# Optimization experiments

Measured on AMD Instinct MI355X. Metric: run time of the kernel, lower is better.

Reference implementation:

```python
import jax, jax.numpy as jnp
import numpy as np

B, S, D = 4, 2048, 768
H = 12
HD = D // H  # 64


def setup_inputs() -> dict:
    key = jax.random.key(0)
    k1, k2, k3 = jax.random.split(key, 3)
    return {
        "hidden_states": jax.random.normal(k1, (B, S, D), dtype=jnp.float32),
        "W_attn": jax.random.normal(k2, (D, 3 * D), dtype=jnp.float32) * 0.02,
        "b_attn": jnp.zeros((3 * D,), dtype=jnp.float32),
        "W_proj": jax.random.normal(k3, (D, D), dtype=jnp.float32) * 0.02,
        "b_proj": jnp.zeros((D,), dtype=jnp.float32),
    }


def reference(hidden_states, W_attn, b_attn, W_proj, b_proj):
    # Conv1D c_attn: x @ W + b -> [B, S, 3D]
    qkv = hidden_states @ W_attn + b_attn
    q, k, v = jnp.split(qkv, 3, axis=-1)

    def split_heads(t):
        # [B, S, D] -> [B, H, S, HD]
        return t.reshape(B, S, H, HD).transpose(0, 2, 1, 3)

    q, k, v = split_heads(q), split_heads(k), split_heads(v)

    # attn_weights = q @ k^T / sqrt(head_dim); NOTE: this module variant applies
    # no causal mask when attention_mask is None (faithful to source _attn).
    scale = jnp.asarray(HD, dtype=q.dtype) ** 0.5
    scores = jnp.einsum("bhqd,bhkd->bhqk", q, k) / scale
    weights = jax.nn.softmax(scores, axis=-1)

    attn = jnp.einsum("bhqk,bhkd->bhqd", weights, v)
    # merge heads -> [B, S, D]
    attn = attn.transpose(0, 2, 1, 3).reshape(B, S, D)
    # Conv1D c_proj
    out = attn @ W_proj + b_proj
    return out
```

## Files before the change

### kernel.cpp

```cpp
#include <hip/hip_runtime.h>

typedef short short8 __attribute__((ext_vector_type(8)));
typedef float f32x2 __attribute__((ext_vector_type(2)));
typedef float f32x4 __attribute__((ext_vector_type(4)));
typedef float f32x16 __attribute__((ext_vector_type(16)));

__device__ __forceinline__ unsigned short f2bf(float f){
  union { float f; unsigned int u; } x; x.f = f;
  unsigned int r = x.u + 0x7fffu + ((x.u >> 16) & 1u);
  return (unsigned short)(r >> 16);
}

__device__ __forceinline__ void gload_lds16(const void* g, void* l){
  __builtin_amdgcn_global_load_lds(
      (const __attribute__((address_space(1))) void*)g,
      (__attribute__((address_space(3))) void*)l, 16, 0, 0);
}

__device__ __forceinline__ unsigned int cvtpk_bf16(float lo, float hi){
  unsigned int r;
  asm("v_cvt_pk_bf16_f32 %0, %1, %2" : "=v"(r) : "v"(lo), "v"(hi));
  return r;
}

__device__ __forceinline__ f32x2 pk_add(f32x2 a, f32x2 b){
  f32x2 d;
  asm("v_pk_add_f32 %0, %1, %2" : "=v"(d) : "v"(a), "v"(b));
  return d;
}

__global__ __launch_bounds__(256) void prep_fused(const float* __restrict__ hs,
                                                  unsigned short* __restrict__ hbf,
                                                  const float* __restrict__ Wa,
                                                  unsigned short* __restrict__ WaT,
                                                  const float* __restrict__ Wp,
                                                  unsigned short* __restrict__ WpT){
  __shared__ float tile[64][68];
  const int b = blockIdx.x;
  const int t = threadIdx.x;
  if (b < 2048){
    const int n4 = 8192 * 768 / 4;
    int i = b * 256 + t;
    for (; i < n4; i += 2048 * 256){
      float4 v = ((const float4*)hs)[i];
      ushort4 o;
      o.x = f2bf(v.x); o.y = f2bf(v.y); o.z = f2bf(v.z); o.w = f2bf(v.w);
      ((ushort4*)hbf)[i] = o;
    }
    return;
  }
  const float* W; unsigned short* WT; int K, N, n0, k0;
  if (b < 2480){
    const int idx = b - 2048;
    W = Wa; WT = WaT; K = 768; N = 2304;
    n0 = (idx % 36) * 64; k0 = (idx / 36) * 64;
  } else {
    const int idx = b - 2480;
    W = Wp; WT = WpT; K = 768; N = 768;
    n0 = (idx % 12) * 64; k0 = (idx / 12) * 64;
  }
  const int qn = (t & 15) * 4;
  #pragma unroll
  for (int i = 0; i < 4; ++i){
    const int kk = (t >> 4) + i * 16;
    float4 v = *(const float4*)&W[(size_t)(k0 + kk) * N + n0 + qn];
    tile[kk][qn + 0] = v.x; tile[kk][qn + 1] = v.y;
    tile[kk][qn + 2] = v.z; tile[kk][qn + 3] = v.w;
  }
  __syncthreads();
  const int qk = (t & 15) * 4;
  #pragma unroll
  for (int i = 0; i < 4; ++i){
    const int nn = (t >> 4) + i * 16;
    ushort4 o;
    o.x = f2bf(tile[qk + 0][nn]); o.y = f2bf(tile[qk + 1][nn]);
    o.z = f2bf(tile[qk + 2][nn]); o.w = f2bf(tile[qk + 3][nn]);
    *(ushort4*)&WT[(size_t)(n0 + nn) * K + k0 + qk] = o;
  }
}

__global__ __launch_bounds__(256) void gemm_qkv(const unsigned short* __restrict__ A,
                                                const unsigned short* __restrict__ Bt,
                                                const float* __restrict__ bias,
                                                unsigned short* __restrict__ qkv){
  __shared__ unsigned short As[2][128 * 32];
  __shared__ unsigned short Bs[2][128 * 32];
  const int tid = threadIdx.x;
  const int wave = tid >> 6, lane = tid & 63;
  const int g = lane >> 4, l15 = lane & 15;
  const int wr = wave >> 1, wc = wave & 1;
  const int d = blockIdx.x;
  const int w = (d & 7) * 144 + (d >> 3);
  const int m0 = (w / 18) * 128, n0 = (w % 18) * 128;

  f32x4 acc[4][4] = {};

  auto stage = [&](int bi, int kt){
    const int k0 = kt * 32;
    #pragma unroll
    for (int c = 0; c < 2; ++c){
      const int z = c * 4096 + tid * 16;
      const int r = z >> 6;
      const int ys = (z & 63) ^ ((r & 3) << 4);
      gload_lds16((const char*)A + ((size_t)(m0 + r) * 768 + k0) * 2 + ys,
                  (char*)&As[bi][0] + c * 4096 + wave * 1024);
      gload_lds16((const char*)Bt + ((size_t)(n0 + r) * 768 + k0) * 2 + ys,
                  (char*)&Bs[bi][0] + c * 4096 + wave * 1024);
    }
  };

  stage(0, 0);
  for (int kt = 0; kt < 24; ++kt){
    __syncthreads();
    if (kt + 1 < 24) stage((kt + 1) & 1, kt + 1);
    const char* Ab = (const char*)&As[kt & 1][0];
    const char* Bb = (const char*)&Bs[kt & 1][0];
    short8 a[4], b[4];
    #pragma unroll
    for (int mt = 0; mt < 4; ++mt){
      const int row = wr * 64 + mt * 16 + l15;
      a[mt] = *(const short8*)(Ab + row * 64 + ((g * 16) ^ ((row & 3) << 4)));
    }
    #pragma unroll
    for (int nt = 0; nt < 4; ++nt){
      const int row = wc * 64 + nt * 16 + l15;
      b[nt] = *(const short8*)(Bb + row * 64 + ((g * 16) ^ ((row & 3) << 4)));
    }
    #pragma unroll
    for (int mt = 0; mt < 4; ++mt)
      #pragma unroll
      for (int nt = 0; nt < 4; ++nt)
        acc[mt][nt] = __builtin_amdgcn_mfma_f32_16x16x32_bf16(a[mt], b[nt], acc[mt][nt], 0, 0, 0);
  }

  #pragma unroll
  for (int nt = 0; nt < 4; ++nt){
    const int n = n0 + wc * 64 + nt * 16 + l15;
    const int which = n / 768;
    const float bs = bias[n];
    if (which == 2){
      const int hd = n & 63;
      const int head = (n - 1536) >> 6;
      #pragma unroll
      for (int mt = 0; mt < 4; ++mt){
        const int m = m0 + wr * 64 + mt * 16 + 4 * g;
        const int bb = m >> 11, sidx = m & 2047;
        unsigned short* dst = qkv + (size_t)2 * 6291456 +
                              ((size_t)(bb * 12 + head) * 64 + hd) * 2048 + sidx;
        #pragma unroll
        for (int rp = 0; rp < 2; ++rp){
          const unsigned int lo = f2bf(acc[mt][nt][2 * rp] + bs);
          const unsigned int hi = f2bf(acc[mt][nt][2 * rp + 1] + bs);
          *(unsigned int*)(dst + 2 * rp) = lo | (hi << 16);
        }
      }
    } else {
      const int h2 = (n - which * 768) >> 6;
      const int hd = n & 63;
      const float sc = (which == 0) ? 0.18033688f : 1.0f;
      #pragma unroll
      for (int mt = 0; mt < 4; ++mt)
        #pragma unroll
        for (int r = 0; r < 4; ++r){
          const int m = m0 + wr * 64 + mt * 16 + 4 * g + r;
          const int bb = m >> 11, sidx = m & 2047;
          qkv[(size_t)which * 6291456u +
              ((((size_t)bb * 12 + h2) * 2048 + sidx) * 64 + hd)] = f2bf((acc[mt][nt][r] + bs) * sc);
        }
    }
  }
}

__global__ __launch_bounds__(256) void gemm_proj(const unsigned short* __restrict__ A,
                                                 const unsigned short* __restrict__ Bt,
                                                 const float* __restrict__ bias,
                                                 float* __restrict__ out){
  __shared__ unsigned short As[2][128 * 32];
  __shared__ unsigned short Bs[2][64 * 32];
  const int tid = threadIdx.x;
  const int wave = tid >> 6, lane = tid & 63;
  const int g = lane >> 4, l15 = lane & 15;
  const int d = blockIdx.x;
  const int w = (d & 7) * 96 + (d >> 3);
  const int m0 = (w / 12) * 128, n0 = (w % 12) * 64;

  f32x4 acc[2][4] = {};

  auto stage = [&](int bi, int kt){
    const int k0 = kt * 32;
    #pragma unroll
    for (int c = 0; c < 2; ++c){
      const int z = c * 4096 + tid * 16;
      const int r = z >> 6;
      const int ys = (z & 63) ^ ((r & 3) << 4);
      gload_lds16((const char*)A + ((size_t)(m0 + r) * 768 + k0) * 2 + ys,
                  (char*)&As[bi][0] + c * 4096 + wave * 1024);
    }
    const int z = tid * 16;
    const int r = z >> 6;
    const int ys = (z & 63) ^ ((r & 3) << 4);
    gload_lds16((const char*)Bt + ((size_t)(n0 + r) * 768 + k0) * 2 + ys,
                (char*)&Bs[bi][0] + wave * 1024);
  };

  stage(0, 0);
  for (int kt = 0; kt < 24; ++kt){
    __syncthreads();
    if (kt + 1 < 24) stage((kt + 1) & 1, kt + 1);
    const char* Ab = (const char*)&As[kt & 1][0];
    const char* Bb = (const char*)&Bs[kt & 1][0];
    short8 a[2], b[4];
    #pragma unroll
    for (int mt = 0; mt < 2; ++mt){
      const int row = wave * 32 + mt * 16 + l15;
      a[mt] = *(const short8*)(Ab + row * 64 + ((g * 16) ^ ((row & 3) << 4)));
    }
    #pragma unroll
    for (int nt = 0; nt < 4; ++nt){
      const int row = nt * 16 + l15;
      b[nt] = *(const short8*)(Bb + row * 64 + ((g * 16) ^ ((row & 3) << 4)));
    }
    #pragma unroll
    for (int mt = 0; mt < 2; ++mt)
      #pragma unroll
      for (int nt = 0; nt < 4; ++nt)
        acc[mt][nt] = __builtin_amdgcn_mfma_f32_16x16x32_bf16(a[mt], b[nt], acc[mt][nt], 0, 0, 0);
  }

  #pragma unroll
  for (int mt = 0; mt < 2; ++mt)
    #pragma unroll
    for (int nt = 0; nt < 4; ++nt){
      const int n = n0 + nt * 16 + l15;
      const float bs = bias[n];
      #pragma unroll
      for (int r = 0; r < 4; ++r){
        const int m = m0 + wave * 32 + mt * 16 + 4 * g + r;
        out[(size_t)m * 768 + n] = acc[mt][nt][r] + bs;
      }
    }
}

__global__ __launch_bounds__(256) void attn_fwd7(const unsigned short* __restrict__ qw,
                                                 const unsigned short* __restrict__ kw,
                                                 const unsigned short* __restrict__ vtw,
                                                 unsigned short* __restrict__ aout){
  __shared__ unsigned short Ks[2][64 * 64];
  __shared__ unsigned short Vs[2][64 * 64];
  const int tid = threadIdx.x;
  const int wave = tid >> 6, lane = tid & 63;
  const int h = lane >> 5, ql = lane & 31;
  const int dd = blockIdx.x;
  const int wk = (dd & 7) * 96 + (dd >> 3);
  const int bh = wk >> 4;
  const int q0 = (wk & 15) * 128 + wave * 32;
  const size_t base = (size_t)bh * 2048 * 64;

  short8 qf[4];
  #pragma unroll
  for (int c = 0; c < 4; ++c)
    qf[c] = *(const short8*)(qw + base + (size_t)(q0 + ql) * 64 + c * 16 + h * 8);

  f32x16 acc[2] = {};
  float lsum = 0.f;

  auto stageKV = [&](int bi, int t){
    #pragma unroll
    for (int c = 0; c < 2; ++c){
      const int z = c * 4096 + tid * 16;
      const int r = z >> 7, y = z & 127;
      const int ys = y ^ ((r & 7) << 4);
      gload_lds16((const char*)kw + (base + (size_t)(t * 64 + r) * 64) * 2 + ys,
                  (char*)&Ks[bi][0] + z);
      gload_lds16((const char*)vtw + (base + (size_t)r * 2048 + t * 64) * 2 + ys,
                  (char*)&Vs[bi][0] + z);
    }
  };

  stageKV(0, 0);
  __syncthreads();

  for (int t = 0; t < 32; ++t){
    const int buf = t & 1;
    if (t + 1 < 32) stageKV(buf ^ 1, t + 1);

    f32x16 s[2] = {};
    #pragma unroll
    for (int kt = 0; kt < 2; ++kt)
      #pragma unroll
      for (int c = 0; c < 4; ++c){
        const int row = kt * 32 + ql;
        short8 af = *(const short8*)((const char*)&Ks[buf][0] + row * 128 +
                                     ((c * 32 + h * 16) ^ ((row & 7) << 4)));
        s[kt] = __builtin_amdgcn_mfma_f32_32x32x16_bf16(af, qf[c], s[kt], 0, 0, 0);
      }

    #pragma unroll
    for (int kt = 0; kt < 2; ++kt)
      #pragma unroll
      for (int r = 0; r < 16; ++r)
        s[kt][r] = __builtin_amdgcn_exp2f(s[kt][r]);

    {
      f32x2 a0 = pk_add(__builtin_shufflevector(s[0], s[0], 0, 1),  __builtin_shufflevector(s[0], s[0], 2, 3));
      f32x2 a1 = pk_add(__builtin_shufflevector(s[0], s[0], 4, 5),  __builtin_shufflevector(s[0], s[0], 6, 7));
      f32x2 a2 = pk_add(__builtin_shufflevector(s[0], s[0], 8, 9),  __builtin_shufflevector(s[0], s[0], 10, 11));
      f32x2 a3 = pk_add(__builtin_shufflevector(s[0], s[0], 12, 13), __builtin_shufflevector(s[0], s[0], 14, 15));
      f32x2 b0 = pk_add(__builtin_shufflevector(s[1], s[1], 0, 1),  __builtin_shufflevector(s[1], s[1], 2, 3));
      f32x2 b1 = pk_add(__builtin_shufflevector(s[1], s[1], 4, 5),  __builtin_shufflevector(s[1], s[1], 6, 7));
      f32x2 b2 = pk_add(__builtin_shufflevector(s[1], s[1], 8, 9),  __builtin_shufflevector(s[1], s[1], 10, 11));
      f32x2 b3 = pk_add(__builtin_shufflevector(s[1], s[1], 12, 13), __builtin_shufflevector(s[1], s[1], 14, 15));
      a0 = pk_add(a0, a1); a2 = pk_add(a2, a3);
      b0 = pk_add(b0, b1); b2 = pk_add(b2, b3);
      a0 = pk_add(a0, a2); b0 = pk_add(b0, b2);
      a0 = pk_add(a0, b0);
      lsum += a0[0] + a0[1];
    }

    #pragma unroll
    for (int kt = 0; kt < 2; ++kt){
      unsigned int w0 = cvtpk_bf16(s[kt][0],  s[kt][1]),  x0 = cvtpk_bf16(s[kt][4],  s[kt][5]);
      asm("v_permlane32_swap_b32 %0, %1" : "+v"(w0), "+v"(x0));
      unsigned int w1 = cvtpk_bf16(s[kt][2],  s[kt][3]),  x1 = cvtpk_bf16(s[kt][6],  s[kt][7]);
      asm("v_permlane32_swap_b32 %0, %1" : "+v"(w1), "+v"(x1));
      unsigned int w2 = cvtpk_bf16(s[kt][8],  s[kt][9]),  x2 = cvtpk_bf16(s[kt][12], s[kt][13]);
      asm("v_permlane32_swap_b32 %0, %1" : "+v"(w2), "+v"(x2));
      unsigned int w3 = cvtpk_bf16(s[kt][10], s[kt][11]), x3 = cvtpk_bf16(s[kt][14], s[kt][15]);
      asm("v_permlane32_swap_b32 %0, %1" : "+v"(w3), "+v"(x3));
      union { unsigned int u[4]; short8 v; } pa2[2];
      pa2[0].u[0] = w0; pa2[0].u[1] = w1; pa2[0].u[2] = x0; pa2[0].u[3] = x1;
      pa2[1].u[0] = w2; pa2[1].u[1] = w3; pa2[1].u[2] = x2; pa2[1].u[3] = x3;
      #pragma unroll
      for (int c2 = 0; c2 < 2; ++c2){
        const int kc = kt * 2 + c2;
        #pragma unroll
        for (int ht = 0; ht < 2; ++ht){
          const int row = ht * 32 + ql;
          short8 vb = *(const short8*)((const char*)&Vs[buf][0] + row * 128 +
                                       ((kc * 32 + h * 16) ^ ((row & 7) << 4)));
          acc[ht] = __builtin_amdgcn_mfma_f32_32x32x16_bf16(pa2[c2].v, vb, acc[ht], 0, 0, 0);
        }
      }
    }

    __syncthreads();
  }

  lsum += __shfl_xor(lsum, 32);
  const float inv = 1.0f / lsum;
  const int bb = bh / 12, hh = bh % 12;
  #pragma unroll
  for (int g4 = 0; g4 < 4; ++g4)
    #pragma unroll
    for (int j = 0; j < 4; ++j){
      const int row = 8 * g4 + 4 * h + j;
      const float li = __shfl(inv, row);
      #pragma unroll
      for (int ht = 0; ht < 2; ++ht)
        aout[(size_t)(bb * 2048 + q0 + row) * 768 + hh * 64 + ht * 32 + ql] =
            f2bf(acc[ht][4 * g4 + j] * li);
    }
}

extern "C" void kernel_launch(void* const* d_in, const int* in_sizes, int n_in,
                              void* d_out, int out_size, void* d_ws, size_t ws_size,
                              hipStream_t stream){
  const float* hs = (const float*)d_in[0];
  const float* Wa = (const float*)d_in[1];
  const float* ba = (const float*)d_in[2];
  const float* Wp = (const float*)d_in[3];
  const float* bp = (const float*)d_in[4];

  char* ws = (char*)d_ws;
  unsigned short* hbf = (unsigned short*)ws;
  unsigned short* WaT = (unsigned short*)(ws + 12582912);
  unsigned short* WpT = (unsigned short*)(ws + 12582912 + 3538944);
  unsigned short* qkv = (unsigned short*)(ws + 12582912 + 3538944 + 1179648);
  unsigned short* abf = qkv + (size_t)3 * 6291456;

  prep_fused<<<dim3(2624), dim3(256), 0, stream>>>(hs, hbf, Wa, WaT, Wp, WpT);
  gemm_qkv<<<dim3(1152), dim3(256), 0, stream>>>(hbf, WaT, ba, qkv);
  attn_fwd7<<<dim3(768), dim3(256), 0, stream>>>(qkv, qkv + 6291456, qkv + (size_t)2 * 6291456, abf);
  gemm_proj<<<dim3(768), dim3(256), 0, stream>>>(abf, WpT, bp, (float*)d_out);
}
```

Measured before the change: 151.6 us.

## Split QKV GEMM into QK and transposed-output V kernels, change LDS swizzle

The fused QKV projection is split into a Q/K GEMM and a separate V GEMM. The V GEMM swaps operand roles so the accumulator comes out transposed, which lets the transposed V layout be written along the sequence dimension with contiguous lanes. The attention kernel's K/V LDS swizzle now XORs in higher row bits to reduce bank conflicts. The cost is an extra kernel launch, and the V path now does scalar 2-byte stores instead of packed 4-byte stores.

```diff
diff --git a/kernel.cpp b/kernel.cpp
--- a/kernel.cpp
+++ b/kernel.cpp
@@ -27,6 +27,10 @@
   f32x2 d;
   asm("v_pk_add_f32 %0, %1, %2" : "=v"(d) : "v"(a), "v"(b));
   return d;
+}
+
+__device__ __forceinline__ int kvswz(int r){
+  return (((r & 7) ^ ((r >> 3) & 7)) << 4);
 }
 
 __global__ __launch_bounds__(256) void prep_fused(const float* __restrict__ hs,
@@ -79,10 +83,10 @@
   }
 }
 
-__global__ __launch_bounds__(256) void gemm_qkv(const unsigned short* __restrict__ A,
-                                                const unsigned short* __restrict__ Bt,
-                                                const float* __restrict__ bias,
-                                                unsigned short* __restrict__ qkv){
+__global__ __launch_bounds__(256) void gemm_qk(const unsigned short* __restrict__ A,
+                                               const unsigned short* __restrict__ Bt,
+                                               const float* __restrict__ bias,
+                                               unsigned short* __restrict__ qkv){
   __shared__ unsigned short As[2][128 * 32];
   __shared__ unsigned short Bs[2][128 * 32];
   const int tid = threadIdx.x;
@@ -90,8 +94,8 @@
   const int g = lane >> 4, l15 = lane & 15;
   const int wr = wave >> 1, wc = wave & 1;
   const int d = blockIdx.x;
-  const int w = (d & 7) * 144 + (d >> 3);
-  const int m0 = (w / 18) * 128, n0 = (w % 18) * 128;
+  const int w = (d & 7) * 96 + (d >> 3);
+  const int m0 = (w / 12) * 128, n0 = (w % 12) * 128;
 
   f32x4 acc[4][4] = {};
 
@@ -136,39 +140,94 @@
   #pragma unroll
   for (int nt = 0; nt < 4; ++nt){
     const int n = n0 + wc * 64 + nt * 16 + l15;
-    const int which = n / 768;
+    const int which = n >> 9 >= 1 && n >= 768 ? 1 : 0;
     const float bs = bias[n];
-    if (which == 2){
+    const int h2 = (n - which * 768) >> 6;
+    const int hd = n & 63;
+    const float sc = (which == 0) ? 0.18033688f : 1.0f;
+    #pragma unroll
+    for (int mt = 0; mt < 4; ++mt)
+      #pragma unroll
+      for (int r = 0; r < 4; ++r){
+        const int m = m0 + wr * 64 + mt * 16 + 4 * g + r;
+        const int bb = m >> 11, sidx = m & 2047;
+        qkv[(size_t)which * 6291456u +
+            ((((size_t)bb * 12 + h2) * 2048 + sidx) * 64 + hd)] = f2bf((acc[mt][nt][r] + bs) * sc);
+      }
+  }
+}
+
+__global__ __launch_bounds__(256) void gemm_v(const unsigned short* __restrict__ A,
+                                              const unsigned short* __restrict__ Bt,
+                                              const float* __restrict__ bias,
+                                              unsigned short* __restrict__ qkv){
+  __shared__ unsigned short As[2][128 * 32];
+  __shared__ unsigned short Bs[2][128 * 32];
+  const int tid = threadIdx.x;
+  const int wave = tid >> 6, lane = tid & 63;
+  const int g = lane >> 4, l15 = lane & 15;
+  const int wr = wave >> 1, wc = wave & 1;
+  const int d = blockIdx.x;
+  const int w = (d & 7) * 48 + (d >> 3);
+  const int m0 = (w / 6) * 128, n0 = 1536 + (w % 6) * 128;
+
+  f32x4 acc[4][4] = {};
+
+  auto stage = [&](int bi, int kt){
+    const int k0 = kt * 32;
+    #pragma unroll
+    for (int c = 0; c < 2; ++c){
+      const int z = c * 4096 + tid * 16;
+      const int r = z >> 6;
+      const int ys = (z & 63) ^ ((r & 3) << 4);
+      gload_lds16((const char*)A + ((size_t)(m0 + r) * 768 + k0) * 2 + ys,
+                  (char*)&As[bi][0] + c * 4096 + wave * 1024);
+      gload_lds16((const char*)Bt + ((size_t)(n0 + r) * 768 + k0) * 2 + ys,
+                  (char*)&Bs[bi][0] + c * 4096 + wave * 1024);
+    }
+  };
+
+  stage(0, 0);
+  for (int kt = 0; kt < 24; ++kt){
+    __syncthreads();
+    if (kt + 1 < 24) stage((kt + 1) & 1, kt + 1);
+    const char* Ab = (const char*)&As[kt & 1][0];
+    const char* Bb = (const char*)&Bs[kt & 1][0];
+    short8 aw[4], bx[4];
+    #pragma unroll
+    for (int nt = 0; nt < 4; ++nt){
+      const int row = wr * 64 + nt * 16 + l15;
+      aw[nt] = *(const short8*)(Bb + row * 64 + ((g * 16) ^ ((row & 3) << 4)));
+    }
+    #pragma unroll
+    for (int mt = 0; mt < 4; ++mt){
+      const int row = wc * 64 + mt * 16 + l15;
+      bx[mt] = *(const short8*)(Ab + row * 64 + ((g * 16) ^ ((row & 3) << 4)));
+    }
+    #pragma unroll
+    for (int nt = 0; nt < 4; ++nt)
+      #pragma unroll
+      for (int mt = 0; mt < 4; ++mt)
+        acc[nt][mt] = __builtin_amdgcn_mfma_f32_16x16x32_bf16(aw[nt], bx[mt], acc[nt][mt], 0, 0, 0);
+  }
+
+  unsigned short* vbase = qkv + (size_t)2 * 6291456;
+  const int bb = m0 >> 11;
+  #pragma unroll
+  for (int nt = 0; nt < 4; ++nt)
+    #pragma unroll
+    for (int r = 0; r < 4; ++r){
+      const int n = n0 + wr * 64 + nt * 16 + 4 * g + r;
       const int hd = n & 63;
       const int head = (n - 1536) >> 6;
+      const float bs = bias[n];
+      unsigned short* dst = vbase + ((size_t)(bb * 12 + head) * 64 + hd) * 2048;
       #pragma unroll
       for (int mt = 0; mt < 4; ++mt){
-        const int m = m0 + wr * 64 + mt * 16 + 4 * g;
-        const int bb = m >> 11, sidx = m & 2047;
-        unsigned short* dst = qkv + (size_t)2 * 6291456 +
-                              ((size_t)(bb * 12 + head) * 64 + hd) * 2048 + sidx;
-        #pragma unroll
-        for (int rp = 0; rp < 2; ++rp){
-          const unsigned int lo = f2bf(acc[mt][nt][2 * rp] + bs);
-          const unsigned int hi = f2bf(acc[mt][nt][2 * rp + 1] + bs);
-          *(unsigned int*)(dst + 2 * rp) = lo | (hi << 16);
-        }
+        const int m = m0 + wc * 64 + mt * 16 + l15;
+        dst[m & 2047] = f2bf(acc[nt][mt][r] + bs);
       }
-    } else {
-      const int h2 = (n - which * 768) >> 6;
-      const int hd = n & 63;
-      const float sc = (which == 0) ? 0.18033688f : 1.0f;
-      #pragma unroll
-      for (int mt = 0; mt < 4; ++mt)
-        #pragma unroll
-        for (int r = 0; r < 4; ++r){
-          const int m = m0 + wr * 64 + mt * 16 + 4 * g + r;
-          const int bb = m >> 11, sidx = m & 2047;
-          qkv[(size_t)which * 6291456u +
-              ((((size_t)bb * 12 + h2) * 2048 + sidx) * 64 + hd)] = f2bf((acc[mt][nt][r] + bs) * sc);
-        }
-    }
-  }
+    }
 }
 
 __global__ __launch_bounds__(256) void gemm_proj(const unsigned short* __restrict__ A,
@@ -241,7 +300,7 @@
     }
 }
 
-__global__ __launch_bounds__(256) void attn_fwd7(const unsigned short* __restrict__ qw,
+__global__ __launch_bounds__(256) void attn_fwd8(const unsigned short* __restrict__ qw,
                                                  const unsigned short* __restrict__ kw,
                                                  const unsigned short* __restrict__ vtw,
                                                  unsigned short* __restrict__ aout){
@@ -269,7 +328,7 @@
     for (int c = 0; c < 2; ++c){
       const int z = c * 4096 + tid * 16;
       const int r = z >> 7, y = z & 127;
-      const int ys = y ^ ((r & 7) << 4);
+      const int ys = y ^ kvswz(r);
       gload_lds16((const char*)kw + (base + (size_t)(t * 64 + r) * 64) * 2 + ys,
                   (char*)&Ks[bi][0] + z);
       gload_lds16((const char*)vtw + (base + (size_t)r * 2048 + t * 64) * 2 + ys,
@@ -291,7 +350,7 @@
       for (int c = 0; c < 4; ++c){
         const int row = kt * 32 + ql;
         short8 af = *(const short8*)((const char*)&Ks[buf][0] + row * 128 +
-                                     ((c * 32 + h * 16) ^ ((row & 7) << 4)));
+                                     ((c * 32 + h * 16) ^ kvswz(row)));
         s[kt] = __builtin_amdgcn_mfma_f32_32x32x16_bf16(af, qf[c], s[kt], 0, 0, 0);
       }
 
@@ -337,7 +396,7 @@
         for (int ht = 0; ht < 2; ++ht){
           const int row = ht * 32 + ql;
           short8 vb = *(const short8*)((const char*)&Vs[buf][0] + row * 128 +
-                                       ((kc * 32 + h * 16) ^ ((row & 7) << 4)));
+                                       ((kc * 32 + h * 16) ^ kvswz(row)));
           acc[ht] = __builtin_amdgcn_mfma_f32_32x32x16_bf16(pa2[c2].v, vb, acc[ht], 0, 0, 0);
         }
       }
@@ -379,7 +438,8 @@
   unsigned short* abf = qkv + (size_t)3 * 6291456;
 
   prep_fused<<<dim3(2624), dim3(256), 0, stream>>>(hs, hbf, Wa, WaT, Wp, WpT);
-  gemm_qkv<<<dim3(1152), dim3(256), 0, stream>>>(hbf, WaT, ba, qkv);
-  attn_fwd7<<<dim3(768), dim3(256), 0, stream>>>(qkv, qkv + 6291456, qkv + (size_t)2 * 6291456, abf);
+  gemm_qk<<<dim3(768), dim3(256), 0, stream>>>(hbf, WaT, ba, qkv);
+  gemm_v<<<dim3(384), dim3(256), 0, stream>>>(hbf, WaT, ba, qkv);
+  attn_fwd8<<<dim3(768), dim3(256), 0, stream>>>(qkv, qkv + 6291456, qkv + (size_t)2 * 6291456, abf);
   gemm_proj<<<dim3(768), dim3(256), 0, stream>>>(abf, WpT, bp, (float*)d_out);
 }
```

New measurement: 168.0 us. 1.11x slower.
